# Performance work log

Measured on AMD Instinct MI355X. Metric: run time of the kernel, lower is better.

## Reference

```python
import jax, jax.numpy as jnp
import numpy as np

N_NODES = 50000
N_EDGES = 800000
D_IN, D_H, D_Z = 128, 128, 64


def setup_inputs() -> dict:
    key = jax.random.key(0)
    k0, k1, k2, k3, k4 = jax.random.split(key, 5)
    x = jax.random.normal(k0, (N_NODES, D_IN), dtype=jnp.float32)
    edge_index = jax.random.randint(k1, (2, N_EDGES), 0, N_NODES)
    # SAGEConv fc_neigh weights (out_feats, in_feats), bias=False
    W1 = jax.random.normal(k2, (D_H, D_IN), dtype=jnp.float32) / np.sqrt(D_IN)
    W2 = jax.random.normal(k3, (D_H, D_H), dtype=jnp.float32) / np.sqrt(D_H)
    W3 = jax.random.normal(k4, (D_Z, D_H), dtype=jnp.float32) / np.sqrt(D_H)
    return {"x": x, "edge_index": edge_index, "W1": W1, "W2": W2, "W3": W3}


def reference(x, edge_index, W1, W2, W3):
    src, dst = edge_index[0], edge_index[1]
    n = x.shape[0]
    # 'gcn' aggregator: (sum of neighbor feats + self feat) / (in_degree + 1)
    deg = jax.ops.segment_sum(jnp.ones((src.shape[0],), dtype=x.dtype), dst,
                              num_segments=n)
    inv = 1.0 / (deg + 1.0)  # [N]

    def sage_gcn(h, W):
        agg = jax.ops.segment_sum(h[src], dst, num_segments=n) + h  # [N, d_in]
        return (agg * inv[:, None]) @ W.T  # [N, d_out]

    # dropout=0 -> identity; batchnorm in the original is applied to x and
    # discarded, so it never affects h.
    h = jax.nn.relu(sage_gcn(x, W1))
    h = jax.nn.relu(sage_gcn(h, W2))
    h = sage_gcn(h, W3)
    return jax.nn.relu(h)
```

## Files before the change

### kernel.cpp

```cpp
#include <hip/hip_runtime.h>

#define N_NODES 50000
#define N_EDGES 800000
#define D 128


__global__ void deg_wtrans_kernel(const int* __restrict__ dst, int* __restrict__ deg,
                                  const float* __restrict__ W1, const float* __restrict__ W2,
                                  const float* __restrict__ W3, float* __restrict__ wT) {
  int b = blockIdx.x;
  if (b < 3125) {
    int e = b * 256 + threadIdx.x;
    if (e < N_EDGES) atomicAdd(&deg[dst[e]], 1);
  } else {
    int g = (b - 3125) * 256 + threadIdx.x;
    if (g < 16384) {
      int k = g >> 7, o = g & 127;
      wT[g] = W1[o * 128 + k];
    } else if (g < 32768) {
      int l = g - 16384;
      int k = l >> 7, o = l & 127;
      wT[g] = W2[o * 128 + k];
    } else if (g < 40960) {
      int l = g - 32768;
      int k = l >> 6, o = l & 63;
      wT[g] = W3[o * 128 + k];
    }
  }
}

__global__ void scan_kernel(const int* __restrict__ deg, int* __restrict__ row_start,
                            int* __restrict__ cursor, float* __restrict__ inv) {
  __shared__ int wsum[16];
  __shared__ int carry_s;
  const int t = threadIdx.x;
  const int lane = t & 63, wid = t >> 6;
  if (t == 0) carry_s = 0;
  __syncthreads();
  for (int base = 0; base < N_NODES; base += 4096) {
    int i0 = base + t * 4;
    int v[4];
    int s = 0;
#pragma unroll
    for (int j = 0; j < 4; ++j) {
      int i = i0 + j;
      v[j] = (i < N_NODES) ? deg[i] : 0;
      s += v[j];
    }
    int run = s;
#pragma unroll
    for (int off = 1; off < 64; off <<= 1) {
      int o = __shfl_up(run, off);
      if (lane >= off) run += o;
    }
    if (lane == 63) wsum[wid] = run;
    __syncthreads();
    if (t < 16) {
      int w = wsum[t];
#pragma unroll
      for (int off = 1; off < 16; off <<= 1) {
        int o = __shfl_up(w, off, 16);
        if (t >= off) w += o;
      }
      wsum[t] = w;
    }
    __syncthreads();
    int excl = carry_s + (wid ? wsum[wid - 1] : 0) + run - s;
#pragma unroll
    for (int j = 0; j < 4; ++j) {
      int i = i0 + j;
      if (i < N_NODES) {
        row_start[i] = excl;
        cursor[i] = excl;
        inv[i] = 1.0f / (float)(v[j] + 1);
      }
      excl += v[j];
    }
    __syncthreads();
    if (t == 0) carry_s += wsum[15];
    __syncthreads();
  }
  if (t == 0) row_start[N_NODES] = carry_s;
}

__global__ void csr_kernel(const int* __restrict__ src, const int* __restrict__ dst,
                           int* __restrict__ cursor, int* __restrict__ csr) {
  int e = blockIdx.x * 256 + threadIdx.x;
  if (e < N_EDGES) {
    int p = atomicAdd(&cursor[dst[e]], 1);
    csr[p] = src[e];
  }
}


template <int DV, bool RELU>
__global__ __launch_bounds__(256) void agg_kernel(const float* __restrict__ G,
    const int* __restrict__ row_start, const int* __restrict__ csr,
    const float* __restrict__ inv, float* __restrict__ outA) {
  constexpr int L = DV / 4;
  constexpr int NPW = 64 / L;
  const int wave = (blockIdx.x * 256 + threadIdx.x) >> 6;
  const int lane = threadIdx.x & 63;
  const int sub = lane / L;
  const int li = lane % L;
  const int node = wave * NPW + sub;

  const float4* hp = (const float4*)G;
  float4 acc = hp[(size_t)node * L + li];
  float4 acc2 = make_float4(0.f, 0.f, 0.f, 0.f);
  const int s = row_start[node], e = row_start[node + 1];
  int j = s;
  for (; j + 8 <= e; j += 8) {
    int n0 = csr[j + 0], n1 = csr[j + 1], n2 = csr[j + 2], n3 = csr[j + 3];
    int n4 = csr[j + 4], n5 = csr[j + 5], n6 = csr[j + 6], n7 = csr[j + 7];
    float4 v0 = hp[(size_t)n0 * L + li];
    float4 v1 = hp[(size_t)n1 * L + li];
    float4 v2 = hp[(size_t)n2 * L + li];
    float4 v3 = hp[(size_t)n3 * L + li];
    float4 v4 = hp[(size_t)n4 * L + li];
    float4 v5 = hp[(size_t)n5 * L + li];
    float4 v6 = hp[(size_t)n6 * L + li];
    float4 v7 = hp[(size_t)n7 * L + li];
    acc.x  += (v0.x + v1.x) + (v2.x + v3.x);
    acc.y  += (v0.y + v1.y) + (v2.y + v3.y);
    acc.z  += (v0.z + v1.z) + (v2.z + v3.z);
    acc.w  += (v0.w + v1.w) + (v2.w + v3.w);
    acc2.x += (v4.x + v5.x) + (v6.x + v7.x);
    acc2.y += (v4.y + v5.y) + (v6.y + v7.y);
    acc2.z += (v4.z + v5.z) + (v6.z + v7.z);
    acc2.w += (v4.w + v5.w) + (v6.w + v7.w);
  }
  for (; j + 4 <= e; j += 4) {
    int n0 = csr[j + 0], n1 = csr[j + 1], n2 = csr[j + 2], n3 = csr[j + 3];
    float4 v0 = hp[(size_t)n0 * L + li];
    float4 v1 = hp[(size_t)n1 * L + li];
    float4 v2 = hp[(size_t)n2 * L + li];
    float4 v3 = hp[(size_t)n3 * L + li];
    acc.x += (v0.x + v1.x) + (v2.x + v3.x);
    acc.y += (v0.y + v1.y) + (v2.y + v3.y);
    acc.z += (v0.z + v1.z) + (v2.z + v3.z);
    acc.w += (v0.w + v1.w) + (v2.w + v3.w);
  }
  for (; j < e; ++j) {
    int nb = csr[j];
    float4 v = hp[(size_t)nb * L + li];
    acc2.x += v.x; acc2.y += v.y; acc2.z += v.z; acc2.w += v.w;
  }
  acc.x += acc2.x; acc.y += acc2.y; acc.z += acc2.z; acc.w += acc2.w;
  float iv = inv[node];
  acc.x *= iv; acc.y *= iv; acc.z *= iv; acc.w *= iv;
  if (RELU) {
    acc.x = fmaxf(acc.x, 0.f); acc.y = fmaxf(acc.y, 0.f);
    acc.z = fmaxf(acc.z, 0.f); acc.w = fmaxf(acc.w, 0.f);
  }
  ((float4*)outA)[(size_t)node * L + li] = acc;
}

template <int DOUT>
__global__ __launch_bounds__(256, 2) void gemm_kernel(const float* __restrict__ A,
    const float* __restrict__ wT, float* __restrict__ out) {
  constexpr int TO = DOUT / 16;
  __shared__ float aL[128 * 64];
  __shared__ float wL[64 * DOUT];
  const int t = threadIdx.x;
  const int row0 = blockIdx.x * 128;

  const int w = t >> 6, l = t & 63;
  const int rowT = (l >> 3) + ((w >> 1) << 3);
  const int outT = (l & 7) + ((w & 1) << 3);

  const float4* A4 = (const float4*)A;
  const float4* w4 = (const float4*)wT;
  float4* aL4 = (float4*)aL;
  float4* wL4 = (float4*)wL;
  const float4* aL4c = (const float4*)aL;
  const float4* wL4c = (const float4*)wL;

  float acc[8][TO];
#pragma unroll
  for (int i = 0; i < 8; ++i)
#pragma unroll
    for (int j = 0; j < TO; ++j) acc[i][j] = 0.f;

#define DK_STEP(COMP, DK)                                                  \
  {                                                                        \
    _Pragma("unroll")                                                      \
    for (int j4 = 0; j4 < TO / 4; ++j4) {                                  \
      float4 b = wL4c[(kb * 4 + (DK)) * (DOUT / 4) + outT * (TO / 4) + j4];\
      _Pragma("unroll")                                                    \
      for (int i = 0; i < 8; ++i) {                                        \
        float av = a[i].COMP;                                              \
        acc[i][j4 * 4 + 0] += av * b.x;                                    \
        acc[i][j4 * 4 + 1] += av * b.y;                                    \
        acc[i][j4 * 4 + 2] += av * b.z;                                    \
        acc[i][j4 * 4 + 3] += av * b.w;                                    \
      }                                                                    \
    }                                                                      \
  }

#pragma unroll
  for (int kt = 0; kt < 2; ++kt) {
    if (kt) __syncthreads();
#pragma unroll
    for (int i = 0; i < 8; ++i) {
      int g4 = t + i * 256;
      int r = g4 >> 4;
      int k4 = g4 & 15;
      int gr = row0 + r;
      float4 v = make_float4(0.f, 0.f, 0.f, 0.f);
      if (gr < N_NODES) v = A4[(size_t)gr * 32 + kt * 16 + k4];
      aL4[r * 16 + (k4 ^ ((r >> 3) & 15))] = v;
    }
#pragma unroll
    for (int i = 0; i < TO; ++i) {
      int g4 = t + i * 256;
      int k = g4 / (DOUT / 4);
      int o4 = g4 % (DOUT / 4);
      wL4[k * (DOUT / 4) + o4] = w4[(size_t)(kt * 64 + k) * (DOUT / 4) + o4];
    }
    __syncthreads();

    for (int kb = 0; kb < 16; ++kb) {
      float4 a[8];
#pragma unroll
      for (int i = 0; i < 8; ++i)
        a[i] = aL4c[(rowT * 8 + i) * 16 + (kb ^ rowT)];
      DK_STEP(x, 0)
      DK_STEP(y, 1)
      DK_STEP(z, 2)
      DK_STEP(w, 3)
    }
  }
#undef DK_STEP

#pragma unroll
  for (int i = 0; i < 8; ++i) {
    int gr = row0 + rowT * 8 + i;
    if (gr < N_NODES) {
#pragma unroll
      for (int j4 = 0; j4 < TO / 4; ++j4) {
        float4 v = make_float4(acc[i][j4 * 4 + 0], acc[i][j4 * 4 + 1],
                               acc[i][j4 * 4 + 2], acc[i][j4 * 4 + 3]);
        *(float4*)&out[(size_t)gr * DOUT + outT * TO + j4 * 4] = v;
      }
    }
  }
}


extern "C" void kernel_launch(void* const* d_in, const int* in_sizes, int n_in,
                              void* d_out, int out_size, void* d_ws, size_t ws_size,
                              hipStream_t stream) {
  const float* x  = (const float*)d_in[0];
  const int* ei   = (const int*)d_in[1];
  const float* W1 = (const float*)d_in[2];
  const float* W2 = (const float*)d_in[3];
  const float* W3 = (const float*)d_in[4];
  const int* src = ei;
  const int* dst = ei + N_EDGES;
  float* out = (float*)d_out;

  char* ws = (char*)d_ws;
  size_t off = 0;
  auto alloc = [&](size_t bytes) {
    void* p = ws + off;
    off += (bytes + 255) & ~(size_t)255;
    return p;
  };
  int* deg       = (int*)alloc(N_NODES * sizeof(int));
  int* row_start = (int*)alloc((N_NODES + 1) * sizeof(int));
  int* cursor    = (int*)alloc(N_NODES * sizeof(int));
  int* csr       = (int*)alloc(N_EDGES * sizeof(int));
  float* inv     = (float*)alloc(N_NODES * sizeof(float));
  float* wT      = (float*)alloc((16384 + 16384 + 8192) * sizeof(float));
  float* G       = (float*)alloc((size_t)N_NODES * D * sizeof(float));
  float* H       = (float*)alloc((size_t)N_NODES * D * sizeof(float));
  (void)ws_size;

  float* wT1 = wT;
  float* wT2 = wT + 16384;
  float* wT3 = wT + 32768;

  hipMemsetAsync(deg, 0, N_NODES * sizeof(int), stream);

  const int eblocks = (N_EDGES + 255) / 256;
  deg_wtrans_kernel<<<eblocks + 160, 256, 0, stream>>>(dst, deg, W1, W2, W3, wT);
  scan_kernel<<<1, 1024, 0, stream>>>(deg, row_start, cursor, inv);
  csr_kernel<<<eblocks, 256, 0, stream>>>(src, dst, cursor, csr);

  const int gblocks = (N_NODES + 127) / 128;

  gemm_kernel<128><<<gblocks, 256, 0, stream>>>(x, wT1, G);
  agg_kernel<128, true><<<6250, 256, 0, stream>>>(G, row_start, csr, inv, H);
  gemm_kernel<128><<<gblocks, 256, 0, stream>>>(H, wT2, G);
  agg_kernel<128, true><<<6250, 256, 0, stream>>>(G, row_start, csr, inv, H);
  gemm_kernel<64><<<gblocks, 256, 0, stream>>>(H, wT3, G);
  agg_kernel<64, true><<<3125, 256, 0, stream>>>(G, row_start, csr, inv, out);
}
```

Before: 446.8 us.

## Fuse first-layer GEMM into degree/transpose kernel and single-pass scan

```diff
diff --git a/kernel.cpp b/kernel.cpp
--- a/kernel.cpp
+++ b/kernel.cpp
@@ -4,83 +4,176 @@
 #define N_EDGES 800000
 #define D 128
 
-
-__global__ void deg_wtrans_kernel(const int* __restrict__ dst, int* __restrict__ deg,
-                                  const float* __restrict__ W1, const float* __restrict__ W2,
-                                  const float* __restrict__ W3, float* __restrict__ wT) {
-  int b = blockIdx.x;
-  if (b < 3125) {
-    int e = b * 256 + threadIdx.x;
+__global__ __launch_bounds__(256, 2) void fused_gemm1_kernel(
+    const float* __restrict__ x, const float* __restrict__ W1,
+    const int* __restrict__ dst, int* __restrict__ deg,
+    const float* __restrict__ W2, const float* __restrict__ W3,
+    float* __restrict__ wT, float* __restrict__ G) {
+  __shared__ float aL[128 * 64];
+  __shared__ float wL[64 * 128];
+  const int b = blockIdx.x;
+  const int t = threadIdx.x;
+
+  if (b < 391) {
+    const int row0 = b * 128;
+    const int w = t >> 6, l = t & 63;
+    const int rowT = (l >> 3) + ((w >> 1) << 3);
+    const int outT = (l & 7) + ((w & 1) << 3);
+
+    const float4* A4 = (const float4*)x;
+    float4* aL4 = (float4*)aL;
+    float4* wL4 = (float4*)wL;
+    const float4* aL4c = (const float4*)aL;
+    const float4* wL4c = (const float4*)wL;
+
+    float acc[8][8];
+#pragma unroll
+    for (int i = 0; i < 8; ++i)
+#pragma unroll
+      for (int j = 0; j < 8; ++j) acc[i][j] = 0.f;
+
+#define DK_STEP1(COMP, DK)                                              \
+  {                                                                     \
+    _Pragma("unroll")                                                   \
+    for (int j4 = 0; j4 < 2; ++j4) {                                    \
+      float4 bb = wL4c[(kb * 4 + (DK)) * 32 + outT * 2 + j4];           \
+      _Pragma("unroll")                                                 \
+      for (int i = 0; i < 8; ++i) {                                     \
+        float av = a[i].COMP;                                           \
+        acc[i][j4 * 4 + 0] += av * bb.x;                                \
+        acc[i][j4 * 4 + 1] += av * bb.y;                                \
+        acc[i][j4 * 4 + 2] += av * bb.z;                                \
+        acc[i][j4 * 4 + 3] += av * bb.w;                                \
+      }                                                                 \
+    }                                                                   \
+  }
+
+#pragma unroll
+    for (int kt = 0; kt < 2; ++kt) {
+      if (kt) __syncthreads();
+#pragma unroll
+      for (int i = 0; i < 8; ++i) {
+        int g4 = t + i * 256;
+        int r = g4 >> 4;
+        int k4 = g4 & 15;
+        int gr = row0 + r;
+        float4 v = make_float4(0.f, 0.f, 0.f, 0.f);
+        if (gr < N_NODES) v = A4[(size_t)gr * 32 + kt * 16 + k4];
+        aL4[r * 16 + (k4 ^ ((r >> 3) & 15))] = v;
+      }
+#pragma unroll
+      for (int i = 0; i < 8; ++i) {
+        int g4 = t + i * 256;
+        int k = g4 >> 5;
+        int o4 = g4 & 31;
+        int kk = kt * 64 + k;
+        int o = o4 * 4;
+        float4 v = make_float4(W1[(o + 0) * 128 + kk], W1[(o + 1) * 128 + kk],
+                               W1[(o + 2) * 128 + kk], W1[(o + 3) * 128 + kk]);
+        wL4[k * 32 + o4] = v;
+      }
+      __syncthreads();
+
+      for (int kb = 0; kb < 16; ++kb) {
+        float4 a[8];
+#pragma unroll
+        for (int i = 0; i < 8; ++i)
+          a[i] = aL4c[(rowT * 8 + i) * 16 + (kb ^ rowT)];
+        DK_STEP1(x, 0)
+        DK_STEP1(y, 1)
+        DK_STEP1(z, 2)
+        DK_STEP1(w, 3)
+      }
+    }
+#undef DK_STEP1
+
+#pragma unroll
+    for (int i = 0; i < 8; ++i) {
+      int gr = row0 + rowT * 8 + i;
+      if (gr < N_NODES) {
+#pragma unroll
+        for (int j4 = 0; j4 < 2; ++j4) {
+          float4 v = make_float4(acc[i][j4 * 4 + 0], acc[i][j4 * 4 + 1],
+                                 acc[i][j4 * 4 + 2], acc[i][j4 * 4 + 3]);
+          *(float4*)&G[(size_t)gr * 128 + outT * 8 + j4 * 4] = v;
+        }
+      }
+    }
+  } else if (b < 3516) {
+    int e = (b - 391) * 256 + t;
     if (e < N_EDGES) atomicAdd(&deg[dst[e]], 1);
   } else {
-    int g = (b - 3125) * 256 + threadIdx.x;
+    int g = (b - 3516) * 256 + t;
     if (g < 16384) {
       int k = g >> 7, o = g & 127;
-      wT[g] = W1[o * 128 + k];
-    } else if (g < 32768) {
+      wT[16384 + g] = W2[o * 128 + k];
+    } else if (g < 24576) {
       int l = g - 16384;
-      int k = l >> 7, o = l & 127;
-      wT[g] = W2[o * 128 + k];
-    } else if (g < 40960) {
-      int l = g - 32768;
       int k = l >> 6, o = l & 63;
-      wT[g] = W3[o * 128 + k];
-    }
-  }
-}
+      wT[32768 + l] = W3[o * 128 + k];
+    }
+  }
+}
+
 
 __global__ void scan_kernel(const int* __restrict__ deg, int* __restrict__ row_start,
                             int* __restrict__ cursor, float* __restrict__ inv) {
   __shared__ int wsum[16];
-  __shared__ int carry_s;
   const int t = threadIdx.x;
   const int lane = t & 63, wid = t >> 6;
-  if (t == 0) carry_s = 0;
+  const int i0 = t * 52;
+  const int4* d4 = (const int4*)deg;
+  int s = 0;
+  if (i0 + 52 <= N_NODES) {
+#pragma unroll
+    for (int j = 0; j < 13; ++j) {
+      int4 v = d4[i0 / 4 + j];
+      s += (v.x + v.y) + (v.z + v.w);
+    }
+  } else {
+    for (int i = i0; i < N_NODES; ++i) s += deg[i];
+  }
+  int run = s;
+#pragma unroll
+  for (int off = 1; off < 64; off <<= 1) {
+    int o = __shfl_up(run, off);
+    if (lane >= off) run += o;
+  }
+  if (lane == 63) wsum[wid] = run;
   __syncthreads();
-  for (int base = 0; base < N_NODES; base += 4096) {
-    int i0 = base + t * 4;
-    int v[4];
-    int s = 0;
-#pragma unroll
-    for (int j = 0; j < 4; ++j) {
-      int i = i0 + j;
-      v[j] = (i < N_NODES) ? deg[i] : 0;
-      s += v[j];
-    }
-    int run = s;
-#pragma unroll
-    for (int off = 1; off < 64; off <<= 1) {
-      int o = __shfl_up(run, off);
-      if (lane >= off) run += o;
-    }
-    if (lane == 63) wsum[wid] = run;
-    __syncthreads();
-    if (t < 16) {
-      int w = wsum[t];
-#pragma unroll
-      for (int off = 1; off < 16; off <<= 1) {
-        int o = __shfl_up(w, off, 16);
-        if (t >= off) w += o;
-      }
-      wsum[t] = w;
-    }
-    __syncthreads();
-    int excl = carry_s + (wid ? wsum[wid - 1] : 0) + run - s;
-#pragma unroll
-    for (int j = 0; j < 4; ++j) {
-      int i = i0 + j;
-      if (i < N_NODES) {
-        row_start[i] = excl;
-        cursor[i] = excl;
-        inv[i] = 1.0f / (float)(v[j] + 1);
-      }
-      excl += v[j];
-    }
-    __syncthreads();
-    if (t == 0) carry_s += wsum[15];
-    __syncthreads();
-  }
-  if (t == 0) row_start[N_NODES] = carry_s;
+  if (t < 16) {
+    int w = wsum[t];
+#pragma unroll
+    for (int off = 1; off < 16; off <<= 1) {
+      int o = __shfl_up(w, off, 16);
+      if (t >= off) w += o;
+    }
+    wsum[t] = w;
+  }
+  __syncthreads();
+  int excl = (wid ? wsum[wid - 1] : 0) + run - s;
+  if (i0 + 52 <= N_NODES) {
+#pragma unroll
+    for (int j = 0; j < 13; ++j) {
+      int4 v = d4[i0 / 4 + j];
+      int e0 = excl, e1 = e0 + v.x, e2 = e1 + v.y, e3 = e2 + v.z;
+      ((int4*)row_start)[i0 / 4 + j] = make_int4(e0, e1, e2, e3);
+      ((int4*)cursor)[i0 / 4 + j] = make_int4(e0, e1, e2, e3);
+      ((float4*)inv)[i0 / 4 + j] =
+          make_float4(1.f / (float)(v.x + 1), 1.f / (float)(v.y + 1),
+                      1.f / (float)(v.z + 1), 1.f / (float)(v.w + 1));
+      excl = e3 + v.w;
+    }
+  } else {
+    for (int i = i0; i < N_NODES; ++i) {
+      int d = deg[i];
+      row_start[i] = excl;
+      cursor[i] = excl;
+      inv[i] = 1.f / (float)(d + 1);
+      excl += d;
+    }
+  }
+  if (t == 1023) row_start[N_NODES] = excl;
 }
 
 __global__ void csr_kernel(const int* __restrict__ src, const int* __restrict__ dst,
@@ -277,20 +370,19 @@
   float* H       = (float*)alloc((size_t)N_NODES * D * sizeof(float));
   (void)ws_size;
 
-  float* wT1 = wT;
   float* wT2 = wT + 16384;
   float* wT3 = wT + 32768;
 
   hipMemsetAsync(deg, 0, N_NODES * sizeof(int), stream);
 
   const int eblocks = (N_EDGES + 255) / 256;
-  deg_wtrans_kernel<<<eblocks + 160, 256, 0, stream>>>(dst, deg, W1, W2, W3, wT);
+  fused_gemm1_kernel<<<391 + eblocks + 96, 256, 0, stream>>>(
+      x, W1, dst, deg, W2, W3, wT, G);
   scan_kernel<<<1, 1024, 0, stream>>>(deg, row_start, cursor, inv);
   csr_kernel<<<eblocks, 256, 0, stream>>>(src, dst, cursor, csr);
 
   const int gblocks = (N_NODES + 127) / 128;
 
-  gemm_kernel<128><<<gblocks, 256, 0, stream>>>(x, wT1, G);
   agg_kernel<128, true><<<6250, 256, 0, stream>>>(G, row_start, csr, inv, H);
   gemm_kernel<128><<<gblocks, 256, 0, stream>>>(H, wT2, G);
   agg_kernel<128, true><<<6250, 256, 0, stream>>>(G, row_start, csr, inv, H);
```

Result: faster. 390.0 us (-12.7%).
